# Optimization experiments

Hardware: AMD Instinct MI355X
Metric: run time of the kernel (lower is better)

## Reference

```python
import jax, jax.numpy as jnp
import numpy as np

B, N, D, H, FN, NL = 8, 512, 128, 64, 3, 3
OUT = 10


def setup_inputs() -> dict:
    key = jax.random.key(0)
    ks = jax.random.split(key, 20)
    X = jax.random.normal(ks[0], (B, N, D), dtype=jnp.float32)
    a = jax.random.uniform(ks[1], (B, N, N))
    A = (a < 0.02).astype(jnp.float32)
    A = jnp.maximum(A, jnp.swapaxes(A, 1, 2)) * (1.0 - jnp.eye(N, dtype=jnp.float32))
    w = lambda k, s: jax.random.normal(k, s, dtype=jnp.float32) * 0.05
    z = lambda s: jnp.zeros(s, jnp.float32)
    return {
        'X': X, 'A': A, 'p': 10,
        'curv_W1': w(ks[2], (D, H)), 'curv_b1': z((H,)),
        'curv_W2': w(ks[3], (H, 1)), 'curv_b2': z((1,)),
        'wm_W1': w(ks[4], (1, 64)), 'wm_b1': z((64,)),
        'wm_W2': w(ks[5], (64, 32)), 'wm_b2': z((32,)),
        'wm_W3': w(ks[6], (32, 1)), 'wm_b3': z((1,)),
        'fn_W1': w(ks[7], (FN, D, H)), 'fn_b1': z((FN, H)),
        'fn_W2': w(ks[8], (FN, H, 1)), 'fn_b2': z((FN, 1)),
        'gin_eps': z((NL,)),
        'gin0_W1': w(ks[9], (D, H)), 'gin0_b1': z((H,)),
        'gin0_W2': w(ks[10], (H, H)), 'gin0_b2': z((H,)),
        'gin1_W1': w(ks[11], (H, H)), 'gin1_b1': z((H,)),
        'gin1_W2': w(ks[12], (H, H)), 'gin1_b2': z((H,)),
        'gin2_W1': w(ks[13], (H, H)), 'gin2_b1': z((H,)),
        'gin2_W2': w(ks[14], (H, H)), 'gin2_b2': z((H,)),
        'out_W': w(ks[15], (D + H * NL, OUT)), 'out_b': z((OUT,)),
    }


def _curv_mlp(x, W1, b1, W2, b2):
    # MLP(nfeat->nhid->1) followed by sigmoid
    return jax.nn.sigmoid(jax.nn.relu(x @ W1 + b1) @ W2 + b2)


def _weight_mlp(A, W1, b1, W2, b2, W3, b3):
    # per-entry scalar MLP over adjacency: [B,N,N] -> [B,N,N]
    x = jax.nn.relu(A[..., None] * W1[0] + b1)  # [B,N,N,64]
    x = jax.nn.relu(x @ W2 + b2)                # [B,N,N,32]
    return jax.nn.sigmoid(x @ W3 + b3)[..., 0]


def _mv(w, v):
    return jnp.einsum('bij,bj->bi', w, v)


def _curvature_terms(f, w):
    # Algebraically identical to the torch O(N^2) expanded version, but
    # expressed with matvec contractions to avoid redundant [B,N,N] temps.
    deg = w.sum(axis=2)
    wf = _mv(w, f)
    # gamma_i = 0.5 sum_j w_ij (f_j - f_i)^2
    gamma = 0.5 * (f * f * deg - 2.0 * f * wf + _mv(w, f * f))
    # delta_f_i = sum_j w_ij (f_i - f_j)
    delta_f = f * deg - wf
    # delta_gamma_i = sum_j w_ij (gamma_i - gamma_j)
    delta_gamma = gamma * deg - _mv(w, gamma)
    # gfd_i = 0.5 sum_j w_ij (f_i - f_j)(delta_f_i - delta_f_j)
    gfd = 0.5 * (f * delta_f * deg - f * _mv(w, delta_f)
                 - delta_f * wf + _mv(w, f * delta_f))
    gamma2 = 0.5 * delta_gamma - gfd
    return gamma, gamma2


def _prune(A, kap, pct):
    num = int(N * pct / 100)  # static under jit (pct is a Python int)
    _, idx = jax.lax.top_k(kap, num)
    mask = jnp.ones((B, N), A.dtype).at[jnp.arange(B)[:, None], idx].set(0.0)
    return A * mask[:, :, None] * mask[:, None, :]


def _forward(X, A, curv_W1, curv_b1, curv_W2, curv_b2,
             wm_W1, wm_b1, wm_W2, wm_b2, wm_W3, wm_b3,
             fn_W1, fn_b1, fn_W2, fn_b2, gin_eps,
             gin0_W1, gin0_b1, gin0_W2, gin0_b2,
             gin1_W1, gin1_b1, gin1_W2, gin1_b2,
             gin2_W1, gin2_b1, gin2_W2, gin2_b2,
             out_W, out_b, p):
    kappa = _curv_mlp(X, curv_W1, curv_b1, curv_W2, curv_b2)  # [B,N,1]
    kap = kappa[..., 0]
    weights = _weight_mlp(A, wm_W1, wm_b1, wm_W2, wm_b2, wm_W3, wm_b3) * A
    curv_loss = jnp.float32(0.0)
    for i in range(FN):
        f = _curv_mlp(X, fn_W1[i], fn_b1[i], fn_W2[i], fn_b2[i])[..., 0]
        gamma, gamma2 = _curvature_terms(f, weights)
        curv_loss = curv_loss + jax.nn.relu(kap * gamma - gamma2).sum() - kappa.sum()
    gins = [(gin0_W1, gin0_b1, gin0_W2, gin0_b2),
            (gin1_W1, gin1_b1, gin1_W2, gin1_b2),
            (gin2_W1, gin2_b1, gin2_W2, gin2_b2)]
    h, A_cur, hiddens = X, A, [X]
    for t in range(NL):
        W1, b1, W2, b2 = gins[t]
        # GIN: MLP((1+eps) x + A x); dropout is identity (eval/deterministic)
        agg = (1.0 + gin_eps[t]) * h + jnp.einsum('bij,bjd->bid', A_cur, h)
        h = jax.nn.relu(jax.nn.relu(agg @ W1 + b1) @ W2 + b2)
        A_cur = _prune(A_cur, kap, p * (t + 1))
        hiddens.append(h)
    out = jnp.concatenate(hiddens, axis=2).sum(axis=1) @ out_W + out_b
    return out, curv_loss


def reference(X, A, p, curv_W1, curv_b1, curv_W2, curv_b2,
              wm_W1, wm_b1, wm_W2, wm_b2, wm_W3, wm_b3,
              fn_W1, fn_b1, fn_W2, fn_b2, gin_eps,
              gin0_W1, gin0_b1, gin0_W2, gin0_b2,
              gin1_W1, gin1_b1, gin1_W2, gin1_b2,
              gin2_W1, gin2_b1, gin2_W2, gin2_b2,
              out_W, out_b):
    return _forward(X, A, curv_W1, curv_b1, curv_W2, curv_b2,
                    wm_W1, wm_b1, wm_W2, wm_b2, wm_W3, wm_b3,
                    fn_W1, fn_b1, fn_W2, fn_b2, gin_eps,
                    gin0_W1, gin0_b1, gin0_W2, gin0_b2,
                    gin1_W1, gin1_b1, gin1_W2, gin1_b2,
                    gin2_W1, gin2_b1, gin2_W2, gin2_b2,
                    out_W, out_b, p)
```

## Files before the change

kernel.cpp:

```cpp
#include <hip/hip_runtime.h>
#include <math.h>

#define BATCH 8
#define NNODE 512
#define BN 4096
#define DIM 128
#define HID 64
#define CAP 64

__device__ __forceinline__ float sigmoidf(float x) {
  return 1.f / (1.f + expf(-x));
}
__device__ __forceinline__ float wave_sum(float v) {
  for (int off = 1; off < 64; off <<= 1) v += __shfl_xor(v, off, 64);
  return v;
}

template <int CIN, bool MASKED>
__device__ __forceinline__ void gin_block(
    float* smem, int node0, const float* hin, const float* W1g,
    const float* b1, const float* W2g, const float* b2, float eps1,
    const int* csr, const int* cnt, const float* mask, float* hout) {
  float* W1s = smem;
  float* aggs = smem + CIN * HID;
  float* zs = aggs + 8 * CIN;
  int tid = threadIdx.x, wave = tid >> 6, lane = tid & 63;
  for (int t = tid; t < CIN * HID / 4; t += 256)
    ((float4*)W1s)[t] = ((const float4*)W1g)[t];
  for (int i = 0; i < 2; i++) {
    int ln = wave * 2 + i;
    int r = node0 + ln;
    int b9 = r & ~(NNODE - 1);
    const float* hi = hin + (size_t)r * CIN;
    float a0 = eps1 * hi[lane];
    float a1 = (CIN == 128) ? eps1 * hi[lane + 64] : 0.f;
    int n = cnt[r];
    const int* nb = csr + r * CAP;
    float mrow = MASKED ? mask[r] : 1.f;
    float s0 = 0.f, s1 = 0.f;
    for (int t = 0; t < n; t += 8) {
      int4 ja = *(const int4*)&nb[t];
      int4 jb = *(const int4*)&nb[t + 4];
      int r0 = (r & ~(NNODE - 1)) + ja.x, r1 = b9 + ja.y, r2 = b9 + ja.z,
          r3 = b9 + ja.w;
      int r4 = b9 + jb.x, r5 = b9 + jb.y, r6 = b9 + jb.z, r7 = b9 + jb.w;
      float m0 = MASKED ? mask[r0] : 1.f;
      float m1 = (t + 1 < n) ? (MASKED ? mask[r1] : 1.f) : 0.f;
      float m2 = (t + 2 < n) ? (MASKED ? mask[r2] : 1.f) : 0.f;
      float m3 = (t + 3 < n) ? (MASKED ? mask[r3] : 1.f) : 0.f;
      float m4 = (t + 4 < n) ? (MASKED ? mask[r4] : 1.f) : 0.f;
      float m5 = (t + 5 < n) ? (MASKED ? mask[r5] : 1.f) : 0.f;
      float m6 = (t + 6 < n) ? (MASKED ? mask[r6] : 1.f) : 0.f;
      float m7 = (t + 7 < n) ? (MASKED ? mask[r7] : 1.f) : 0.f;
      const float* p0 = hin + (size_t)r0 * CIN;
      const float* p1 = hin + (size_t)r1 * CIN;
      const float* p2 = hin + (size_t)r2 * CIN;
      const float* p3 = hin + (size_t)r3 * CIN;
      const float* p4 = hin + (size_t)r4 * CIN;
      const float* p5 = hin + (size_t)r5 * CIN;
      const float* p6 = hin + (size_t)r6 * CIN;
      const float* p7 = hin + (size_t)r7 * CIN;
      s0 += m0 * p0[lane] + m1 * p1[lane] + m2 * p2[lane] + m3 * p3[lane] +
            m4 * p4[lane] + m5 * p5[lane] + m6 * p6[lane] + m7 * p7[lane];
      if (CIN == 128)
        s1 += m0 * p0[lane + 64] + m1 * p1[lane + 64] + m2 * p2[lane + 64] +
              m3 * p3[lane + 64] + m4 * p4[lane + 64] + m5 * p5[lane + 64] +
              m6 * p6[lane + 64] + m7 * p7[lane + 64];
    }
    a0 += mrow * s0;
    if (CIN == 128) a1 += mrow * s1;
    aggs[ln * CIN + lane] = a0;
    if (CIN == 128) aggs[ln * CIN + 64 + lane] = a1;
  }
  __syncthreads();
  const float* x0 = aggs + (wave * 2 + 0) * CIN;
  const float* x1 = aggs + (wave * 2 + 1) * CIN;
  float bb = b1[lane];
  float acc0 = bb, acc1 = bb;
  for (int k = 0; k < CIN; k += 4) {
    float w0 = W1s[(k + 0) * HID + lane];
    float w1 = W1s[(k + 1) * HID + lane];
    float w2 = W1s[(k + 2) * HID + lane];
    float w3 = W1s[(k + 3) * HID + lane];
    float4 a;
    a = *(const float4*)&x0[k];
    acc0 += a.x * w0 + a.y * w1 + a.z * w2 + a.w * w3;
    a = *(const float4*)&x1[k];
    acc1 += a.x * w0 + a.y * w1 + a.z * w2 + a.w * w3;
  }
  zs[(wave * 2 + 0) * HID + lane] = fmaxf(0.f, acc0);
  zs[(wave * 2 + 1) * HID + lane] = fmaxf(0.f, acc1);
  const float* z0 = zs + (wave * 2 + 0) * HID;
  const float* z1 = zs + (wave * 2 + 1) * HID;
  float b2b = b2[lane];
  float c0 = b2b, c1v = b2b;
  for (int k = 0; k < HID; k += 4) {
    float w0 = W2g[(k + 0) * HID + lane];
    float w1 = W2g[(k + 1) * HID + lane];
    float w2 = W2g[(k + 2) * HID + lane];
    float w3 = W2g[(k + 3) * HID + lane];
    float4 a;
    a = *(const float4*)&z0[k];
    c0 += a.x * w0 + a.y * w1 + a.z * w2 + a.w * w3;
    a = *(const float4*)&z1[k];
    c1v += a.x * w0 + a.y * w1 + a.z * w2 + a.w * w3;
  }
  size_t rb = (size_t)(node0 + wave * 2) * HID + lane;
  hout[rb + 0 * HID] = fmaxf(0.f, c0);
  hout[rb + 1 * HID] = fmaxf(0.f, c1v);
}

__global__ __launch_bounds__(256) void k_stage1(
    const float* X, const float* A, const float* cW1, const float* cb1,
    const float* cW2, const float* cb2, const float* fW1, const float* fb1,
    const float* fW2, const float* fb2, const float* wm_W1, const float* wm_b1,
    const float* wm_W2, const float* wm_b2, const float* wm_W3,
    const float* wm_b3, float* kap, float* f, float* c1_out, int* csr,
    int* cnt_arr, float* deg) {
  __shared__ float smem[10240];
  int bid = blockIdx.x;
  int tid = threadIdx.x, wave = tid >> 6, lane = tid & 63;
  if (bid < 1024) {
    int m = bid >> 8;
    int grp = bid & 255;
    float* W1s = smem;
    float* xs = smem + 8192;
    int node0 = grp * 16;
    const float* W1 = (m == 0) ? cW1 : fW1 + (size_t)(m - 1) * DIM * HID;
    for (int t = tid; t < 16 * DIM / 4; t += 256)
      ((float4*)xs)[t] = ((const float4*)(X + (size_t)node0 * DIM))[t];
    for (int t = tid; t < DIM * HID / 4; t += 256)
      ((float4*)W1s)[t] = ((const float4*)W1)[t];
    __syncthreads();
    const float* b1 = (m == 0) ? cb1 : fb1 + (m - 1) * HID;
    const float* W2 = (m == 0) ? cW2 : fW2 + (m - 1) * HID;
    float b2v = (m == 0) ? cb2[0] : fb2[m - 1];
    const float* x0 = xs + (wave * 4 + 0) * DIM;
    const float* x1 = xs + (wave * 4 + 1) * DIM;
    const float* x2 = xs + (wave * 4 + 2) * DIM;
    const float* x3 = xs + (wave * 4 + 3) * DIM;
    float w2l = W2[lane];
    float bb = b1[lane];
    float acc0 = bb, acc1 = bb, acc2 = bb, acc3 = bb;
    for (int k = 0; k < DIM; k += 4) {
      float w0 = W1s[(k + 0) * HID + lane];
      float w1 = W1s[(k + 1) * HID + lane];
      float w2 = W1s[(k + 2) * HID + lane];
      float w3 = W1s[(k + 3) * HID + lane];
      float4 a;
      a = *(const float4*)&x0[k];
      acc0 += a.x * w0 + a.y * w1 + a.z * w2 + a.w * w3;
      a = *(const float4*)&x1[k];
      acc1 += a.x * w0 + a.y * w1 + a.z * w2 + a.w * w3;
      a = *(const float4*)&x2[k];
      acc2 += a.x * w0 + a.y * w1 + a.z * w2 + a.w * w3;
      a = *(const float4*)&x3[k];
      acc3 += a.x * w0 + a.y * w1 + a.z * w2 + a.w * w3;
    }
    float s0 = wave_sum(fmaxf(0.f, acc0) * w2l);
    float s1 = wave_sum(fmaxf(0.f, acc1) * w2l);
    float s2 = wave_sum(fmaxf(0.f, acc2) * w2l);
    float s3 = wave_sum(fmaxf(0.f, acc3) * w2l);
    if (lane < 4) {
      float sv = (lane == 0) ? s0 : (lane == 1) ? s1 : (lane == 2) ? s2 : s3;
      float s = sigmoidf(sv + b2v);
      int node = node0 + wave * 4 + lane;
      if (m == 0) kap[node] = s;
      else f[node * 3 + (m - 1)] = s;
    }
    return;
  }
  if (bid < 2048) {
    int r = (bid - 1024) * 4 + wave;
    const float* row = A + (size_t)r * NNODE;
    int base = r * CAP, cnt = 0;
    for (int c = 0; c < NNODE / 64; c++) {
      int j = c * 64 + lane;
      bool nz = (row[j] != 0.f);
      unsigned long long mb = __ballot(nz);
      if (nz) {
        int pos = __popcll(mb & ((1ull << lane) - 1ull));
        int slot = cnt + pos;
        if (slot < CAP) csr[base + slot] = j;
      }
      cnt += (int)__popcll(mb);
    }
    int cc = cnt < CAP ? cnt : CAP;
    if (lane >= cc) csr[base + lane] = 0;
    if (lane == 0) {
      cnt_arr[r] = cc;
      deg[r] = (float)cnt;
    }
    return;
  }
  float* u = smem;
  float* y = smem + 64;
  int l = tid;
  if (l < 64) u[l] = fmaxf(0.f, wm_W1[l] + wm_b1[l]);
  __syncthreads();
  if (l < 32) {
    float a = wm_b2[l];
    for (int k = 0; k < 64; k++) a += u[k] * wm_W2[k * 32 + l];
    y[l] = fmaxf(0.f, a);
  }
  __syncthreads();
  if (l == 0) {
    float a = wm_b3[0];
    for (int k = 0; k < 32; k++) a += y[k] * wm_W3[k];
    *c1_out = sigmoidf(a);
  }
}

__global__ __launch_bounds__(256) void k_stage2(
    const float* X, const float* f, const float* kap, const int* p_ptr,
    const int* csr, const int* cnt, const float* deg, const float* c1p,
    const float* g0_W1, const float* g0_b1, const float* g0_W2,
    const float* g0_b2, const float* gin_eps, float* GG, float* M1, float* M2,
    float* h1) {
  __shared__ float smem[9728];
  int bid = blockIdx.x;
  int wave = threadIdx.x >> 6, lane = threadIdx.x & 63;
  if (bid < 1024) {
    int r = bid * 4 + wave;
    int b9 = r & ~(NNODE - 1);
    int n = cnt[r];
    int j = csr[r * CAP + lane];
    float f0 = 0.f, f1 = 0.f, f2 = 0.f;
    if (lane < n) {
      const float* fj = f + (size_t)(b9 + j) * 3;
      f0 = fj[0]; f1 = fj[1]; f2 = fj[2];
    }
    float s10 = wave_sum(f0), s11 = wave_sum(f1), s12 = wave_sum(f2);
    float s20 = wave_sum(f0 * f0), s21 = wave_sum(f1 * f1),
          s22 = wave_sum(f2 * f2);
    if (lane < 3) {
      float s1 = (lane == 0) ? s10 : (lane == 1) ? s11 : s12;
      float s2 = (lane == 0) ? s20 : (lane == 1) ? s21 : s22;
      float c1 = *c1p, dA = deg[r];
      float fi = f[r * 3 + lane];
      float gamma = 0.5f * c1 * (fi * fi * dA - 2.f * fi * s1 + s2);
      float df = c1 * (fi * dA - s1);
      float* o = GG + (size_t)r * 12;
      o[lane * 3 + 0] = gamma;
      o[lane * 3 + 1] = df;
      o[lane * 3 + 2] = fi * df;
      o[9 + lane] = s1;
    }
    return;
  }
  if (bid < 1024 + BATCH) {
    int b = bid - 1024;
    float* ks = smem;
    for (int t = threadIdx.x; t < NNODE; t += 256) ks[t] = kap[b * NNODE + t];
    __syncthreads();
    int p = *p_ptr;
    int num1 = (NNODE * p) / 100;
    int num2 = (NNODE * 2 * p) / 100;
    int numm = num1 > num2 ? num1 : num2;
    for (int i = threadIdx.x; i < NNODE; i += 256) {
      float v = ks[i];
      int rank = 0;
      for (int j = 0; j < NNODE; j++) {
        float u = ks[j];
        rank += (u > v) || (u == v && j < i);
      }
      M1[b * NNODE + i] = (rank < num1) ? 0.f : 1.f;
      M2[b * NNODE + i] = (rank < numm) ? 0.f : 1.f;
    }
    return;
  }
  gin_block<DIM, false>(smem, (bid - 1024 - BATCH) * 8, X, g0_W1, g0_b1,
                        g0_W2, g0_b2, 1.f + gin_eps[0], csr, cnt, nullptr, h1);
}

__global__ __launch_bounds__(256) void k_stage3(
    const float* f, const float* kap, const float* deg, const float* GG,
    const int* csr, const int* cnt, const float* c1p, float* loss_part,
    const float* h1, const float* g1_W1, const float* g1_b1,
    const float* g1_W2, const float* g1_b2, const float* gin_eps,
    const float* M1, float* h2) {
  __shared__ float smem[5120];
  __shared__ float part[4];
  int bid = blockIdx.x;
  int wave = threadIdx.x >> 6, lane = threadIdx.x & 63;
  if (bid < 1024) {
    int r = bid * 4 + wave;
    int b9 = r & ~(NNODE - 1);
    int n = cnt[r];
    int j = csr[r * CAP + lane];
    float T[9];
    for (int c = 0; c < 9; c++) T[c] = 0.f;
    if (lane < n) {
      const float4* g = (const float4*)(GG + (size_t)(b9 + j) * 12);
      float4 g0 = g[0], g1 = g[1], g2 = g[2];
      T[0] = g0.x; T[1] = g0.y; T[2] = g0.z;
      T[3] = g0.w; T[4] = g1.x; T[5] = g1.y;
      T[6] = g1.z; T[7] = g1.w; T[8] = g2.x;
    }
    for (int c = 0; c < 9; c++) T[c] = wave_sum(T[c]);
    float kp = kap[r];
    float local = 0.f;
    if (lane < 3) {
      int i = lane;
      float c1 = *c1p, dA = deg[r];
      const float* o = GG + (size_t)r * 12;
      float fi = f[r * 3 + i];
      float s1 = o[9 + i];
      float gamma = o[i * 3 + 0], df = o[i * 3 + 1];
      float dgamma = c1 * (gamma * dA - T[i * 3 + 0]);
      float gfd = 0.5f * c1 * (fi * df * dA - fi * T[i * 3 + 1] - df * s1 +
                               T[i * 3 + 2]);
      float gamma2 = 0.5f * dgamma - gfd;
      local = fmaxf(0.f, kp * gamma - gamma2);
    }
    if (lane == 0) local -= 3.f * kp;
    local = wave_sum(local);
    if (lane == 0) part[wave] = local;
    __syncthreads();
    if (threadIdx.x == 0)
      loss_part[bid] = part[0] + part[1] + part[2] + part[3];
    return;
  }
  gin_block<HID, true>(smem, (bid - 1024) * 8, h1, g1_W1, g1_b1, g1_W2, g1_b2,
                       1.f + gin_eps[1], csr, cnt, M1, h2);
}

__global__ __launch_bounds__(256) void k_stage4(
    const float* h2, const float* g2_W1, const float* g2_b1,
    const float* g2_W2, const float* g2_b2, const float* gin_eps,
    const int* csr, const int* cnt, const float* M2, float* h3) {
  __shared__ float smem[5120];
  gin_block<HID, true>(smem, blockIdx.x * 8, h2, g2_W1, g2_b1, g2_W2, g2_b2,
                       1.f + gin_eps[2], csr, cnt, M2, h3);
}

__global__ __launch_bounds__(640) void k_out(
    const float* X, const float* h1, const float* h2, const float* h3,
    const float* out_W, const float* out_b, const float* loss_part,
    float* out) {
  int b = blockIdx.x;
  int t = threadIdx.x;
  __shared__ float S[640];
  __shared__ float wpart[10];
  int half = t / 320, c = t % 320;
  const float* src;
  int C, col;
  if (c < 128)      { src = X  + (size_t)b * NNODE * DIM; C = DIM; col = c; }
  else if (c < 192) { src = h1 + (size_t)b * NNODE * HID; C = HID; col = c - 128; }
  else if (c < 256) { src = h2 + (size_t)b * NNODE * HID; C = HID; col = c - 192; }
  else              { src = h3 + (size_t)b * NNODE * HID; C = HID; col = c - 256; }
  int n0 = half * (NNODE / 2);
  float s = 0.f;
  for (int n = n0; n < n0 + NNODE / 2; n++) s += src[(size_t)n * C + col];
  S[t] = s;
  if (b == 0) {
    float ls = 0.f;
    for (int i = t; i < 1024; i += 640) ls += loss_part[i];
    ls = wave_sum(ls);
    if ((t & 63) == 0) wpart[t >> 6] = ls;
  }
  __syncthreads();
  if (t < 10) {
    float acc = out_b[t];
    for (int d = 0; d < 320; d++)
      acc += (S[d] + S[d + 320]) * out_W[d * 10 + t];
    out[b * 10 + t] = acc;
  }
  if (b == 0 && t == 0) {
    float ls = 0.f;
    for (int w = 0; w < 10; w++) ls += wpart[w];
    out[80] = ls;
  }
}

extern "C" void kernel_launch(void* const* d_in, const int* in_sizes, int n_in,
                              void* d_out, int out_size, void* d_ws,
                              size_t ws_size, hipStream_t stream) {
  const float* X       = (const float*)d_in[0];
  const float* A       = (const float*)d_in[1];
  const int*   p       = (const int*)d_in[2];
  const float* curv_W1 = (const float*)d_in[3];
  const float* curv_b1 = (const float*)d_in[4];
  const float* curv_W2 = (const float*)d_in[5];
  const float* curv_b2 = (const float*)d_in[6];
  const float* wm_W1   = (const float*)d_in[7];
  const float* wm_b1   = (const float*)d_in[8];
  const float* wm_W2   = (const float*)d_in[9];
  const float* wm_b2   = (const float*)d_in[10];
  const float* wm_W3   = (const float*)d_in[11];
  const float* wm_b3   = (const float*)d_in[12];
  const float* fn_W1   = (const float*)d_in[13];
  const float* fn_b1   = (const float*)d_in[14];
  const float* fn_W2   = (const float*)d_in[15];
  const float* fn_b2   = (const float*)d_in[16];
  const float* gin_eps = (const float*)d_in[17];
  const float* g0_W1   = (const float*)d_in[18];
  const float* g0_b1   = (const float*)d_in[19];
  const float* g0_W2   = (const float*)d_in[20];
  const float* g0_b2   = (const float*)d_in[21];
  const float* g1_W1   = (const float*)d_in[22];
  const float* g1_b1   = (const float*)d_in[23];
  const float* g1_W2   = (const float*)d_in[24];
  const float* g1_b2   = (const float*)d_in[25];
  const float* g2_W1   = (const float*)d_in[26];
  const float* g2_b1   = (const float*)d_in[27];
  const float* g2_W2   = (const float*)d_in[28];
  const float* g2_b2   = (const float*)d_in[29];
  const float* out_W   = (const float*)d_in[30];
  const float* out_b   = (const float*)d_in[31];
  float* out = (float*)d_out;

  float* ws = (float*)d_ws;
  size_t o = 0;
  float* loss_part = ws + o; o += 1024;
  float* c1       = ws + o; o += 16;
  float* kap      = ws + o; o += BN;
  float* f        = ws + o; o += (size_t)BN * 3 + 16;
  float* deg      = ws + o; o += BN;
  float* M1       = ws + o; o += BN;
  float* M2       = ws + o; o += BN;
  float* GG       = ws + o; o += (size_t)BN * 12;
  float* h1       = ws + o; o += (size_t)BN * HID;
  float* h2       = ws + o; o += (size_t)BN * HID;
  float* h3       = ws + o; o += (size_t)BN * HID;
  int* cnt  = (int*)(ws + o); o += BN;
  int* csr  = (int*)(ws + o); o += (size_t)BN * CAP;

  k_stage1<<<2049, 256, 0, stream>>>(
      X, A, curv_W1, curv_b1, curv_W2, curv_b2, fn_W1, fn_b1, fn_W2, fn_b2,
      wm_W1, wm_b1, wm_W2, wm_b2, wm_W3, wm_b3, kap, f, c1, csr, cnt, deg);
  k_stage2<<<1024 + BATCH + 512, 256, 0, stream>>>(
      X, f, kap, p, csr, cnt, deg, c1, g0_W1, g0_b1, g0_W2, g0_b2, gin_eps,
      GG, M1, M2, h1);
  k_stage3<<<1536, 256, 0, stream>>>(f, kap, deg, GG, csr, cnt, c1, loss_part,
                                     h1, g1_W1, g1_b1, g1_W2, g1_b2, gin_eps,
                                     M1, h2);
  k_stage4<<<512, 256, 0, stream>>>(h2, g2_W1, g2_b1, g2_W2, g2_b2, gin_eps,
                                    csr, cnt, M2, h3);
  k_out<<<BATCH, 640, 0, stream>>>(X, h1, h2, h3, out_W, out_b, loss_part,
                                   out);
}
```

Measured before the change: 212.9 us.

## Fuse per-graph column sums into GIN blocks with atomics, shrink output kernel

Each GIN block now reduces its output rows into per-batch column sums in shared memory and adds them atomically to a small Ssum buffer. Extra blocks in stage 2 reduce X column sums the same way, and stage 1 zeroes the buffer. The final kernel only reads the 320 precomputed sums per batch instead of rescanning X, h1, h2 and h3 with just 8 blocks, which was a serial tail. The cost is an extra __syncthreads and float atomics in every GIN block, which makes the summation order nondeterministic.

New measurement: 200.5 us. 5.8% less time.

```diff
diff --git a/kernel.cpp b/kernel.cpp
--- a/kernel.cpp
+++ b/kernel.cpp
@@ -16,11 +16,12 @@
   return v;
 }
 
-template <int CIN, bool MASKED>
+template <int CIN, bool MASKED, int SOFF>
 __device__ __forceinline__ void gin_block(
     float* smem, int node0, const float* hin, const float* W1g,
     const float* b1, const float* W2g, const float* b2, float eps1,
-    const int* csr, const int* cnt, const float* mask, float* hout) {
+    const int* csr, const int* cnt, const float* mask, float* hout,
+    float* Ssum) {
   float* W1s = smem;
   float* aggs = smem + CIN * HID;
   float* zs = aggs + 8 * CIN;
@@ -41,8 +42,7 @@
     for (int t = 0; t < n; t += 8) {
       int4 ja = *(const int4*)&nb[t];
       int4 jb = *(const int4*)&nb[t + 4];
-      int r0 = (r & ~(NNODE - 1)) + ja.x, r1 = b9 + ja.y, r2 = b9 + ja.z,
-          r3 = b9 + ja.w;
+      int r0 = b9 + ja.x, r1 = b9 + ja.y, r2 = b9 + ja.z, r3 = b9 + ja.w;
       int r4 = b9 + jb.x, r5 = b9 + jb.y, r6 = b9 + jb.z, r7 = b9 + jb.w;
       float m0 = MASKED ? mask[r0] : 1.f;
       float m1 = (t + 1 < n) ? (MASKED ? mask[r1] : 1.f) : 0.f;
@@ -105,9 +105,17 @@
     a = *(const float4*)&z1[k];
     c1v += a.x * w0 + a.y * w1 + a.z * w2 + a.w * w3;
   }
+  float h0 = fmaxf(0.f, c0), h1v = fmaxf(0.f, c1v);
   size_t rb = (size_t)(node0 + wave * 2) * HID + lane;
-  hout[rb + 0 * HID] = fmaxf(0.f, c0);
-  hout[rb + 1 * HID] = fmaxf(0.f, c1v);
+  hout[rb + 0 * HID] = h0;
+  hout[rb + 1 * HID] = h1v;
+  zs[(wave * 2) * HID + lane] = h0 + h1v;
+  __syncthreads();
+  if (tid < HID) {
+    float tot = zs[0 * HID + tid] + zs[2 * HID + tid] + zs[4 * HID + tid] +
+                zs[6 * HID + tid];
+    atomicAdd(&Ssum[(node0 >> 9) * 320 + SOFF + tid], tot);
+  }
 }
 
 __global__ __launch_bounds__(256) void k_stage1(
@@ -116,7 +124,7 @@
     const float* fW2, const float* fb2, const float* wm_W1, const float* wm_b1,
     const float* wm_W2, const float* wm_b2, const float* wm_W3,
     const float* wm_b3, float* kap, float* f, float* c1_out, int* csr,
-    int* cnt_arr, float* deg) {
+    int* cnt_arr, float* deg, float* Ssum) {
   __shared__ float smem[10240];
   int bid = blockIdx.x;
   int tid = threadIdx.x, wave = tid >> 6, lane = tid & 63;
@@ -193,6 +201,7 @@
     }
     return;
   }
+  for (int t = tid; t < BATCH * 320; t += 256) Ssum[t] = 0.f;
   float* u = smem;
   float* y = smem + 64;
   int l = tid;
@@ -216,7 +225,7 @@
     const int* csr, const int* cnt, const float* deg, const float* c1p,
     const float* g0_W1, const float* g0_b1, const float* g0_W2,
     const float* g0_b2, const float* gin_eps, float* GG, float* M1, float* M2,
-    float* h1) {
+    float* h1, float* Ssum) {
   __shared__ float smem[9728];
   int bid = blockIdx.x;
   int wave = threadIdx.x >> 6, lane = threadIdx.x & 63;
@@ -269,8 +278,23 @@
     }
     return;
   }
-  gin_block<DIM, false>(smem, (bid - 1024 - BATCH) * 8, X, g0_W1, g0_b1,
-                        g0_W2, g0_b2, 1.f + gin_eps[0], csr, cnt, nullptr, h1);
+  if (bid < 1024 + BATCH + 512) {
+    gin_block<DIM, false, 128>(smem, (bid - 1024 - BATCH) * 8, X, g0_W1,
+                               g0_b1, g0_W2, g0_b2, 1.f + gin_eps[0], csr,
+                               cnt, nullptr, h1, Ssum);
+    return;
+  }
+  int idx = bid - (1024 + BATCH + 512);
+  int b = idx >> 3, sl = idx & 7;
+  int col = threadIdx.x & 127, rg = threadIdx.x >> 7;
+  const float* xb = X + (size_t)b * NNODE * DIM;
+  int n0 = sl * 64;
+  float s = 0.f;
+  for (int n = n0 + rg; n < n0 + 64; n += 2) s += xb[(size_t)n * DIM + col];
+  smem[threadIdx.x] = s;
+  __syncthreads();
+  if (threadIdx.x < 128)
+    atomicAdd(&Ssum[b * 320 + col], smem[threadIdx.x] + smem[threadIdx.x + 128]);
 }
 
 __global__ __launch_bounds__(256) void k_stage3(
@@ -278,7 +302,7 @@
     const int* csr, const int* cnt, const float* c1p, float* loss_part,
     const float* h1, const float* g1_W1, const float* g1_b1,
     const float* g1_W2, const float* g1_b2, const float* gin_eps,
-    const float* M1, float* h2) {
+    const float* M1, float* h2, float* Ssum) {
   __shared__ float smem[5120];
   __shared__ float part[4];
   int bid = blockIdx.x;
@@ -321,54 +345,42 @@
       loss_part[bid] = part[0] + part[1] + part[2] + part[3];
     return;
   }
-  gin_block<HID, true>(smem, (bid - 1024) * 8, h1, g1_W1, g1_b1, g1_W2, g1_b2,
-                       1.f + gin_eps[1], csr, cnt, M1, h2);
+  gin_block<HID, true, 192>(smem, (bid - 1024) * 8, h1, g1_W1, g1_b1, g1_W2,
+                            g1_b2, 1.f + gin_eps[1], csr, cnt, M1, h2, Ssum);
 }
 
 __global__ __launch_bounds__(256) void k_stage4(
     const float* h2, const float* g2_W1, const float* g2_b1,
     const float* g2_W2, const float* g2_b2, const float* gin_eps,
-    const int* csr, const int* cnt, const float* M2, float* h3) {
+    const int* csr, const int* cnt, const float* M2, float* h3, float* Ssum) {
   __shared__ float smem[5120];
-  gin_block<HID, true>(smem, blockIdx.x * 8, h2, g2_W1, g2_b1, g2_W2, g2_b2,
-                       1.f + gin_eps[2], csr, cnt, M2, h3);
-}
-
-__global__ __launch_bounds__(640) void k_out(
-    const float* X, const float* h1, const float* h2, const float* h3,
-    const float* out_W, const float* out_b, const float* loss_part,
-    float* out) {
+  gin_block<HID, true, 256>(smem, blockIdx.x * 8, h2, g2_W1, g2_b1, g2_W2,
+                            g2_b2, 1.f + gin_eps[2], csr, cnt, M2, h3, Ssum);
+}
+
+__global__ __launch_bounds__(320) void k_out(
+    const float* Ssum, const float* out_W, const float* out_b,
+    const float* loss_part, float* out) {
   int b = blockIdx.x;
   int t = threadIdx.x;
-  __shared__ float S[640];
-  __shared__ float wpart[10];
-  int half = t / 320, c = t % 320;
-  const float* src;
-  int C, col;
-  if (c < 128)      { src = X  + (size_t)b * NNODE * DIM; C = DIM; col = c; }
-  else if (c < 192) { src = h1 + (size_t)b * NNODE * HID; C = HID; col = c - 128; }
-  else if (c < 256) { src = h2 + (size_t)b * NNODE * HID; C = HID; col = c - 192; }
-  else              { src = h3 + (size_t)b * NNODE * HID; C = HID; col = c - 256; }
-  int n0 = half * (NNODE / 2);
-  float s = 0.f;
-  for (int n = n0; n < n0 + NNODE / 2; n++) s += src[(size_t)n * C + col];
-  S[t] = s;
+  __shared__ float S[320];
+  __shared__ float wpart[5];
+  S[t] = Ssum[b * 320 + t];
   if (b == 0) {
     float ls = 0.f;
-    for (int i = t; i < 1024; i += 640) ls += loss_part[i];
+    for (int i = t; i < 1024; i += 320) ls += loss_part[i];
     ls = wave_sum(ls);
     if ((t & 63) == 0) wpart[t >> 6] = ls;
   }
   __syncthreads();
   if (t < 10) {
     float acc = out_b[t];
-    for (int d = 0; d < 320; d++)
-      acc += (S[d] + S[d + 320]) * out_W[d * 10 + t];
+    for (int d = 0; d < 320; d++) acc += S[d] * out_W[d * 10 + t];
     out[b * 10 + t] = acc;
   }
   if (b == 0 && t == 0) {
     float ls = 0.f;
-    for (int w = 0; w < 10; w++) ls += wpart[w];
+    for (int w = 0; w < 5; w++) ls += wpart[w];
     out[80] = ls;
   }
 }
@@ -414,6 +426,7 @@
   size_t o = 0;
   float* loss_part = ws + o; o += 1024;
   float* c1       = ws + o; o += 16;
+  float* Ssum     = ws + o; o += BATCH * 320 + 16;
   float* kap      = ws + o; o += BN;
   float* f        = ws + o; o += (size_t)BN * 3 + 16;
   float* deg      = ws + o; o += BN;
@@ -428,15 +441,15 @@
 
   k_stage1<<<2049, 256, 0, stream>>>(
       X, A, curv_W1, curv_b1, curv_W2, curv_b2, fn_W1, fn_b1, fn_W2, fn_b2,
-      wm_W1, wm_b1, wm_W2, wm_b2, wm_W3, wm_b3, kap, f, c1, csr, cnt, deg);
-  k_stage2<<<1024 + BATCH + 512, 256, 0, stream>>>(
+      wm_W1, wm_b1, wm_W2, wm_b2, wm_W3, wm_b3, kap, f, c1, csr, cnt, deg,
+      Ssum);
+  k_stage2<<<1024 + BATCH + 512 + 64, 256, 0, stream>>>(
       X, f, kap, p, csr, cnt, deg, c1, g0_W1, g0_b1, g0_W2, g0_b2, gin_eps,
-      GG, M1, M2, h1);
+      GG, M1, M2, h1, Ssum);
   k_stage3<<<1536, 256, 0, stream>>>(f, kap, deg, GG, csr, cnt, c1, loss_part,
                                      h1, g1_W1, g1_b1, g1_W2, g1_b2, gin_eps,
-                                     M1, h2);
+                                     M1, h2, Ssum);
   k_stage4<<<512, 256, 0, stream>>>(h2, g2_W1, g2_b1, g2_W2, g2_b2, gin_eps,
-                                    csr, cnt, M2, h3);
-  k_out<<<BATCH, 640, 0, stream>>>(X, h1, h2, h3, out_W, out_b, loss_part,
-                                   out);
-}
+                                    csr, cnt, M2, h3, Ssum);
+  k_out<<<BATCH, 320, 0, stream>>>(Ssum, out_W, out_b, loss_part, out);
+}
```
